# Kernel tuning notes

Measured on AMD Instinct MI355X. Metric: run time of the kernel, lower is better.

The kernel has to match this reference:

```python
import jax, jax.numpy as jnp
import numpy as np

EMBED_DIM_LIST = [512, 768, 1024]
NUM_HEADS_LIST = [8, 16]
MAX_D_IN = max(EMBED_DIM_LIST)                                        # 1024
MAX_D_OUT = (max(EMBED_DIM_LIST) // min(NUM_HEADS_LIST)) * 3 * max(NUM_HEADS_LIST)  # 6144
BATCH, SEQ = 8, 1024


def _masks():
    # For combo k = (i, j): weight slice is W[:out_k, :in_k] zero-padded to [MAX_D_OUT, MAX_D_IN].
    out_dims = np.array([e // h * 3 * h for e in EMBED_DIM_LIST for h in NUM_HEADS_LIST])  # [K]
    in_dims = np.array([e for e in EMBED_DIM_LIST for h in NUM_HEADS_LIST])                # [K]
    row = (np.arange(MAX_D_OUT)[None, :] < out_dims[:, None]).astype(np.float32)  # [K, D_out]
    col = (np.arange(MAX_D_IN)[None, :] < in_dims[:, None]).astype(np.float32)    # [K, D_in]
    return jnp.asarray(row), jnp.asarray(col)


def setup_inputs() -> dict:
    key = jax.random.key(0)
    k1, k2, k3, k4 = jax.random.split(key, 4)
    K = len(EMBED_DIM_LIST) * len(NUM_HEADS_LIST)
    x = jax.random.normal(k1, (BATCH, SEQ, MAX_D_IN), dtype=jnp.float32)
    weights = jax.random.uniform(k2, (K,), dtype=jnp.float32)
    W = jax.random.normal(k3, (MAX_D_OUT, MAX_D_IN), dtype=jnp.float32) * 0.02
    b = jax.random.normal(k4, (MAX_D_OUT,), dtype=jnp.float32) * 0.02
    return {"x": x, "weights": weights, "W": W, "b": b}


def reference(x, weights, W, b):
    # weights_mix = sum_k weights[k] * pad(W[:out_k, :in_k])
    #             = W * (sum_k weights[k] * row_mask_k[:, None] * col_mask_k[None, :])
    row, col = _masks()                               # [K, D_out], [K, D_in]
    M = jnp.einsum('k,ko,ki->oi', weights, row, col)  # [D_out, D_in] scalar mixing mask
    W_mix = W * M
    b_mix = b * (weights @ row)                       # [D_out]
    # F.linear: x @ W_mix.T + b_mix
    return jnp.einsum('bsi,oi->bso', x, W_mix) + b_mix
```

## Files before the change

### kernel.cpp

```cpp
#include <hip/hip_runtime.h>

typedef unsigned short u16;
typedef __bf16 bf16x8 __attribute__((ext_vector_type(8)));
typedef float f32x4 __attribute__((ext_vector_type(4)));

#define M_DIM 8192
#define K_DIM 1024
#define N_EFF 3072
#define N_FULL 6144
#define BM 128
#define BN 128
#define BK 32

__device__ __forceinline__ u16 f2bf_rne(float f) {
    unsigned u = __float_as_uint(f);
    u += 0x7fffu + ((u >> 16) & 1u);
    return (u16)(u >> 16);
}

__device__ __forceinline__ void gld_lds16(const u16* g, u16* l) {
    __builtin_amdgcn_global_load_lds(
        (const __attribute__((address_space(1))) unsigned int*)g,
        (__attribute__((address_space(3))) unsigned int*)l, 16, 0, 0);
}

__global__ void cvt_x(const float* __restrict__ in, u16* __restrict__ out, int n8) {
    int i = blockIdx.x * 256 + threadIdx.x;
    if (i >= n8) return;
    const float4* p = reinterpret_cast<const float4*>(in) + 2 * (size_t)i;
    float4 a = p[0], b = p[1];
    union { u16 h[8]; uint4 v; } r;
    float vals[8] = {a.x, a.y, a.z, a.w, b.x, b.y, b.z, b.w};
#pragma unroll
    for (int j = 0; j < 8; j++) r.h[j] = f2bf_rne(vals[j]);
    reinterpret_cast<uint4*>(out)[i] = r.v;
}

__global__ void prep_w(const float* __restrict__ W, const float* __restrict__ wt,
                       u16* __restrict__ Wm, int n8) {
    int i = blockIdx.x * 256 + threadIdx.x;
    if (i >= n8) return;
    float w01 = wt[0] + wt[1], w23 = wt[2] + wt[3], w45 = wt[4] + wt[5];
    int o = i >> 7;
    int ib = (i & 127) * 8;
    float s = w45;
    if (o < 2304 && ib < 768) s += w23;
    if (o < 1536 && ib < 512) s += w01;
    const float4* p = reinterpret_cast<const float4*>(W) + 2 * (size_t)i;
    float4 a = p[0], b = p[1];
    union { u16 h[8]; uint4 v; } r;
    float vals[8] = {a.x, a.y, a.z, a.w, b.x, b.y, b.z, b.w};
#pragma unroll
    for (int j = 0; j < 8; j++) r.h[j] = f2bf_rne(vals[j] * s);
    reinterpret_cast<uint4*>(Wm)[i] = r.v;
}

__global__ __launch_bounds__(256, 3) void gemm_bt(
    const u16* __restrict__ A,
    const u16* __restrict__ B,
    const float* __restrict__ bias,
    const float* __restrict__ wt,
    float* __restrict__ C)
{
    __shared__ u16 As[2 * BM * BK];
    __shared__ u16 Bs[2 * BN * BK];

    const int tid  = threadIdx.x;
    const int bx   = blockIdx.x;
    const int by   = blockIdx.y;
    const int lane = tid & 63;
    const int wv   = tid >> 6;
    const int wm   = (wv >> 1) * 64;
    const int wn   = (wv & 1) * 64;

    f32x4 acc[4][4] = {};

    const u16* Ag = A + (size_t)(by * BM) * K_DIM;
    const u16* Bg = B + (size_t)(bx * BN) * K_DIM;

    const int kq  = (lane >> 4) * 8;
    const int r16 = lane & 15;

    for (int kt = 0; kt < K_DIM; kt += 2 * BK) {
        __syncthreads();
#pragma unroll
        for (int u = 0; u < 4; u++) {
            int c  = u * 256 + tid;
            int st = c >> 9;
            int c2 = c & 511;
            int row = c2 >> 2, kc = (c2 & 3) * 8;
            size_t goff = (size_t)row * K_DIM + kt + st * BK + kc;
            gld_lds16(Ag + goff, &As[c * 8]);
            gld_lds16(Bg + goff, &Bs[c * 8]);
        }
        __syncthreads();

#pragma unroll
        for (int st = 0; st < 2; st++) {
            bf16x8 af[4], bf[4];
#pragma unroll
            for (int t = 0; t < 4; t++) {
                af[t] = *reinterpret_cast<const bf16x8*>(
                    &As[st * 4096 + (wm + t * 16 + r16) * BK + kq]);
                bf[t] = *reinterpret_cast<const bf16x8*>(
                    &Bs[st * 4096 + (wn + t * 16 + r16) * BK + kq]);
            }
#pragma unroll
            for (int tm = 0; tm < 4; tm++)
#pragma unroll
                for (int tn = 0; tn < 4; tn++)
                    acc[tm][tn] = __builtin_amdgcn_mfma_f32_16x16x32_bf16(
                        af[tm], bf[tn], acc[tm][tn], 0, 0, 0);
        }
    }

    const float w01 = wt[0] + wt[1], w23 = wt[2] + wt[3], w45 = wt[4] + wt[5];

    const int m0 = by * BM + wm + (lane >> 4) * 4;
    const int n0 = bx * BN + wn + (lane & 15);
#pragma unroll
    for (int tn = 0; tn < 4; tn++) {
        int n = n0 + tn * 16;
        float s = w45 + (n < 2304 ? w23 : 0.f) + (n < 1536 ? w01 : 0.f);
        float bv = bias[n] * s;
#pragma unroll
        for (int tm = 0; tm < 4; tm++) {
            int m = m0 + tm * 16;
#pragma unroll
            for (int r = 0; r < 4; r++)
                __builtin_nontemporal_store(acc[tm][tn][r] + bv,
                    &C[(size_t)(m + r) * N_FULL + n]);
        }
    }

    const f32x4 z = {0.f, 0.f, 0.f, 0.f};
#pragma unroll
    for (int it = 0; it < 16; it++) {
        int lin = it * 256 + tid;
        int row = lin >> 5;
        int c4  = (lin & 31) * 4;
        __builtin_nontemporal_store(z, reinterpret_cast<f32x4*>(
            &C[(size_t)(by * BM + row) * N_FULL + N_EFF + bx * BN + c4]));
    }
}

extern "C" void kernel_launch(void* const* d_in, const int* in_sizes, int n_in,
                              void* d_out, int out_size, void* d_ws, size_t ws_size,
                              hipStream_t stream) {
    const float* x   = (const float*)d_in[0];
    const float* wts = (const float*)d_in[1];
    const float* W   = (const float*)d_in[2];
    const float* b   = (const float*)d_in[3];
    float* out = (float*)d_out;

    u16* xb = (u16*)d_ws;
    u16* Wm = (u16*)((char*)d_ws + 16777216);

    cvt_x <<<4096, 256, 0, stream>>>(x, xb, M_DIM * K_DIM / 8);
    prep_w<<<1536, 256, 0, stream>>>(W, wts, Wm, N_EFF * K_DIM / 8);
    gemm_bt<<<dim3(N_EFF / BN, M_DIM / BM), 256, 0, stream>>>(xb, Wm, b, wts, out);
}
```

Measured before the change: 283.5 us.

## Restructure GEMM into 256x128 tile with triple-buffered async LDS pipeline

The bf16 GEMM moves to 512-thread blocks computing 256x128 tiles with BK=64. Global-to-LDS loads go into a three-stage ring, prefetched two steps ahead with vmcnt-based waits in place of full sync pairs. LDS addresses are XOR-swizzled to avoid bank conflicts, and MFMA sections are wrapped in s_setprio. The aim is to hide load latency and raise arithmetic intensity, at the cost of more LDS per block (about 144KB) and fewer resident blocks.

Result: no change. 286.6 us (+1.1%).

```diff
diff --git a/kernel.cpp b/kernel.cpp
--- a/kernel.cpp
+++ b/kernel.cpp
@@ -8,9 +8,10 @@
 #define K_DIM 1024
 #define N_EFF 3072
 #define N_FULL 6144
-#define BM 128
+#define BM 256
 #define BN 128
-#define BK 32
+#define BK 64
+#define NKT (K_DIM / BK)
 
 __device__ __forceinline__ u16 f2bf_rne(float f) {
     unsigned u = __float_as_uint(f);
@@ -55,15 +56,14 @@
     reinterpret_cast<uint4*>(Wm)[i] = r.v;
 }
 
-__global__ __launch_bounds__(256, 3) void gemm_bt(
+__global__ __launch_bounds__(512, 2) void gemm_bt(
     const u16* __restrict__ A,
     const u16* __restrict__ B,
     const float* __restrict__ bias,
     const float* __restrict__ wt,
     float* __restrict__ C)
 {
-    __shared__ u16 As[2 * BM * BK];
-    __shared__ u16 Bs[2 * BN * BK];
+    __shared__ u16 lds[3][3][8192];
 
     const int tid  = threadIdx.x;
     const int bx   = blockIdx.x;
@@ -73,61 +73,107 @@
     const int wm   = (wv >> 1) * 64;
     const int wn   = (wv & 1) * 64;
 
+    const int c0  = tid, c1 = tid + 512;
+    const int r0c = c0 >> 3, r1c = c1 >> 3;
+    const size_t o0 = (size_t)r0c * 2048 + (((c0 & 7) * 16) ^ ((r0c & 7) << 4));
+    const size_t o1 = (size_t)r1c * 2048 + (((c1 & 7) * 16) ^ ((r1c & 7) << 4));
+    const int l0 = c0 * 8, l1 = c1 * 8;
+
+    const char* Ab = (const char*)(A + (size_t)by * BM * K_DIM);
+    const char* Bb = (const char*)(B + (size_t)bx * BN * K_DIM);
+
+    auto stage_unit = [&](const char* g, u16* l) {
+        gld_lds16((const u16*)(g + o0), l + l0);
+        gld_lds16((const u16*)(g + o1), l + l1);
+    };
+
+    const int r16 = lane & 15;
+    const int sx  = (lane & 7) << 4;
+    const int kq0 = (((lane >> 4) << 4)) ^ sx;
+    const int au  = wm >> 7;
+    const int ar0 = wm & 64;
+
+    int aoff[4], boff[4];
+#pragma unroll
+    for (int q = 0; q < 4; ++q) {
+        aoff[q] = (ar0 + q * 16 + r16) * 128 + kq0;
+        boff[q] = (wn  + q * 16 + r16) * 128 + kq0;
+    }
+
     f32x4 acc[4][4] = {};
 
-    const u16* Ag = A + (size_t)(by * BM) * K_DIM;
-    const u16* Bg = B + (size_t)(bx * BN) * K_DIM;
-
-    const int kq  = (lane >> 4) * 8;
-    const int r16 = lane & 15;
-
-    for (int kt = 0; kt < K_DIM; kt += 2 * BK) {
-        __syncthreads();
-#pragma unroll
-        for (int u = 0; u < 4; u++) {
-            int c  = u * 256 + tid;
-            int st = c >> 9;
-            int c2 = c & 511;
-            int row = c2 >> 2, kc = (c2 & 3) * 8;
-            size_t goff = (size_t)row * K_DIM + kt + st * BK + kc;
-            gld_lds16(Ag + goff, &As[c * 8]);
-            gld_lds16(Bg + goff, &Bs[c * 8]);
-        }
-        __syncthreads();
-
-#pragma unroll
-        for (int st = 0; st < 2; st++) {
-            bf16x8 af[4], bf[4];
-#pragma unroll
-            for (int t = 0; t < 4; t++) {
-                af[t] = *reinterpret_cast<const bf16x8*>(
-                    &As[st * 4096 + (wm + t * 16 + r16) * BK + kq]);
-                bf[t] = *reinterpret_cast<const bf16x8*>(
-                    &Bs[st * 4096 + (wn + t * 16 + r16) * BK + kq]);
-            }
-#pragma unroll
-            for (int tm = 0; tm < 4; tm++)
-#pragma unroll
-                for (int tn = 0; tn < 4; tn++)
-                    acc[tm][tn] = __builtin_amdgcn_mfma_f32_16x16x32_bf16(
-                        af[tm], bf[tn], acc[tm][tn], 0, 0, 0);
-        }
+    stage_unit(Ab,                lds[0][0]);
+    stage_unit(Ab + 262144,       lds[0][1]);
+    stage_unit(Bb,                lds[0][2]);
+    stage_unit(Ab + 128,          lds[1][0]);
+    stage_unit(Ab + 262144 + 128, lds[1][1]);
+    stage_unit(Bb + 128,          lds[1][2]);
+    asm volatile("s_waitcnt vmcnt(6)" ::: "memory");
+    __builtin_amdgcn_s_barrier();
+
+    int bb = 0;
+    for (int t = 0; t < NKT; ++t) {
+        const int sb = (bb == 0) ? 2 : bb - 1;
+        const u16* Au = lds[bb][au];
+        const u16* Bu = lds[bb][2];
+        const char* Akt = Ab + (size_t)(t + 2) * 128;
+        const char* Bkt = Bb + (size_t)(t + 2) * 128;
+        const bool st = (t < NKT - 2);
+        bf16x8 af[4], bf[4];
+
+        if (st) {
+            stage_unit(Akt,          lds[sb][0]);
+            stage_unit(Akt + 262144, lds[sb][1]);
+        }
+#pragma unroll
+        for (int q = 0; q < 4; ++q) {
+            af[q] = *(const bf16x8*)((const char*)Au + aoff[q]);
+            bf[q] = *(const bf16x8*)((const char*)Bu + boff[q]);
+        }
+        __builtin_amdgcn_s_setprio(1);
+#pragma unroll
+        for (int tm = 0; tm < 4; ++tm)
+#pragma unroll
+            for (int tn = 0; tn < 4; ++tn)
+                acc[tm][tn] = __builtin_amdgcn_mfma_f32_16x16x32_bf16(
+                    af[tm], bf[tn], acc[tm][tn], 0, 0, 0);
+        __builtin_amdgcn_s_setprio(0);
+        __builtin_amdgcn_s_barrier();
+
+        if (st) stage_unit(Bkt, lds[sb][2]);
+#pragma unroll
+        for (int q = 0; q < 4; ++q) {
+            af[q] = *(const bf16x8*)((const char*)Au + (aoff[q] ^ 64));
+            bf[q] = *(const bf16x8*)((const char*)Bu + (boff[q] ^ 64));
+        }
+        __builtin_amdgcn_s_setprio(1);
+#pragma unroll
+        for (int tm = 0; tm < 4; ++tm)
+#pragma unroll
+            for (int tn = 0; tn < 4; ++tn)
+                acc[tm][tn] = __builtin_amdgcn_mfma_f32_16x16x32_bf16(
+                    af[tm], bf[tn], acc[tm][tn], 0, 0, 0);
+        __builtin_amdgcn_s_setprio(0);
+        if (st) asm volatile("s_waitcnt vmcnt(6)" ::: "memory");
+        else    asm volatile("s_waitcnt vmcnt(0)" ::: "memory");
+        __builtin_amdgcn_s_barrier();
+
+        bb = (bb == 2) ? 0 : bb + 1;
     }
 
     const float w01 = wt[0] + wt[1], w23 = wt[2] + wt[3], w45 = wt[4] + wt[5];
-
     const int m0 = by * BM + wm + (lane >> 4) * 4;
-    const int n0 = bx * BN + wn + (lane & 15);
-#pragma unroll
-    for (int tn = 0; tn < 4; tn++) {
+    const int n0 = bx * BN + wn + r16;
+#pragma unroll
+    for (int tn = 0; tn < 4; ++tn) {
         int n = n0 + tn * 16;
         float s = w45 + (n < 2304 ? w23 : 0.f) + (n < 1536 ? w01 : 0.f);
         float bv = bias[n] * s;
 #pragma unroll
-        for (int tm = 0; tm < 4; tm++) {
+        for (int tm = 0; tm < 4; ++tm) {
             int m = m0 + tm * 16;
 #pragma unroll
-            for (int r = 0; r < 4; r++)
+            for (int r = 0; r < 4; ++r)
                 __builtin_nontemporal_store(acc[tm][tn][r] + bv,
                     &C[(size_t)(m + r) * N_FULL + n]);
         }
@@ -135,8 +181,8 @@
 
     const f32x4 z = {0.f, 0.f, 0.f, 0.f};
 #pragma unroll
-    for (int it = 0; it < 16; it++) {
-        int lin = it * 256 + tid;
+    for (int it = 0; it < 16; ++it) {
+        int lin = it * 512 + tid;
         int row = lin >> 5;
         int c4  = (lin & 31) * 4;
         __builtin_nontemporal_store(z, reinterpret_cast<f32x4*>(
@@ -158,5 +204,5 @@
 
     cvt_x <<<4096, 256, 0, stream>>>(x, xb, M_DIM * K_DIM / 8);
     prep_w<<<1536, 256, 0, stream>>>(W, wts, Wm, N_EFF * K_DIM / 8);
-    gemm_bt<<<dim3(N_EFF / BN, M_DIM / BM), 256, 0, stream>>>(xb, Wm, b, wts, out);
-}
+    gemm_bt<<<dim3(N_EFF / BN, M_DIM / BM), 512, 0, stream>>>(xb, Wm, b, wts, out);
+}
```
